# Kernel tuning notes

Hardware: AMD Instinct MI355X
Metric: run time of the kernel (lower is better)

The kernel has to match this reference:

```python
import jax, jax.numpy as jnp
import numpy as np

N = 50000
E = 800000
F_IN = 128
HID = 64
HEADS = 4
P = 16384


def setup_inputs() -> dict:
    key = jax.random.key(0)
    ks = jax.random.split(key, 20)
    s = 0.05
    inp = {
        'x': jax.random.normal(ks[0], (N, F_IN), jnp.float32),
        'edge_src': jax.random.randint(ks[1], (E,), 0, N, jnp.int32),
        'edge_dst': jax.random.randint(ks[2], (E,), 0, N, jnp.int32),
        'edge_attr': jax.random.uniform(ks[3], (E, 1), jnp.float32),
        'pair_indices': jax.random.randint(ks[4], (P, 2), 0, N, jnp.int32),
        # conv1: in=F_IN, heads=4, out=HID, edge_dim=1
        'W1': jax.random.normal(ks[5], (F_IN, HEADS * HID), jnp.float32) * s,
        'We1': jax.random.normal(ks[6], (1, HEADS * HID), jnp.float32) * s,
        'as1': jax.random.normal(ks[7], (HEADS, HID), jnp.float32) * s,
        'ad1': jax.random.normal(ks[8], (HEADS, HID), jnp.float32) * s,
        'ae1': jax.random.normal(ks[9], (HEADS, HID), jnp.float32) * s,
        'b1': jnp.zeros((HEADS * HID,), jnp.float32),
        # conv2: in=4*HID, heads=1, out=HID
        'W2': jax.random.normal(ks[10], (HEADS * HID, HID), jnp.float32) * s,
        'We2': jax.random.normal(ks[11], (1, HID), jnp.float32) * s,
        'as2': jax.random.normal(ks[12], (1, HID), jnp.float32) * s,
        'ad2': jax.random.normal(ks[13], (1, HID), jnp.float32) * s,
        'ae2': jax.random.normal(ks[14], (1, HID), jnp.float32) * s,
        'b2': jnp.zeros((HID,), jnp.float32),
        'Wlin': jax.random.normal(ks[15], (2 * HID, 1), jnp.float32) * s,
        'blin': jnp.zeros((1,), jnp.float32),
    }
    return inp


def gat_conv(x, src, dst, edge_attr, W, We, att_src, att_dst, att_edge, bias, heads, C):
    """PyG GATConv (add_self_loops=True, fill_value='mean', negative_slope=0.2, eval mode)."""
    n = x.shape[0]
    # self-loop edge_attr = mean of incoming edge attrs per node
    deg = jax.ops.segment_sum(jnp.ones_like(dst, dtype=edge_attr.dtype), dst, num_segments=n)
    loop_attr = jax.ops.segment_sum(edge_attr, dst, num_segments=n) / jnp.maximum(deg, 1.0)[:, None]
    loop = jnp.arange(n, dtype=src.dtype)
    src_f = jnp.concatenate([src, loop])
    dst_f = jnp.concatenate([dst, loop])
    ea = jnp.concatenate([edge_attr, loop_attr], axis=0)  # [E+N, 1]
    h = (x @ W).reshape(n, heads, C)                      # [N, H, C]
    a_src = (h * att_src).sum(-1)                         # [N, H]
    a_dst = (h * att_dst).sum(-1)
    e = (ea @ We).reshape(-1, heads, C)                   # [E+N, H, C]
    a_edge = (e * att_edge).sum(-1)                       # [E+N, H]
    alpha = jax.nn.leaky_relu(a_src[src_f] + a_dst[dst_f] + a_edge, 0.2)
    amax = jax.ops.segment_max(alpha, dst_f, num_segments=n)
    ex = jnp.exp(alpha - amax[dst_f])
    denom = jax.ops.segment_sum(ex, dst_f, num_segments=n)
    w = ex / denom[dst_f]                                 # segment softmax over dst
    msg = h[src_f] * w[..., None]                         # [E+N, H, C]
    out = jax.ops.segment_sum(msg, dst_f, num_segments=n) # [N, H, C]
    return out.reshape(n, heads * C) + bias


def reference(x, edge_src, edge_dst, edge_attr, pair_indices,
              W1, We1, as1, ad1, ae1, b1,
              W2, We2, as2, ad2, ae2, b2, Wlin, blin):
    # dropout is identity in eval mode
    h1 = jax.nn.elu(gat_conv(x, edge_src, edge_dst, edge_attr,
                             W1, We1, as1, ad1, ae1, b1, HEADS, HID))
    h2 = gat_conv(h1, edge_src, edge_dst, edge_attr,
                  W2, We2, as2, ad2, ae2, b2, 1, HID)
    d1 = h2[pair_indices[:, 0]]
    d2 = h2[pair_indices[:, 1]]
    pf = jnp.concatenate([d1, d2], axis=1)                # [P, 2*HID]
    return jax.nn.sigmoid(pf @ Wlin + blin).reshape(-1)
```

## Files before the change

### kernel.cpp

```cpp
#include <hip/hip_runtime.h>
#include <hip/hip_fp16.h>
#include <math.h>

typedef __attribute__((ext_vector_type(8))) short short8;
typedef __attribute__((ext_vector_type(4))) float floatx4;
typedef __attribute__((ext_vector_type(2))) float float2v;

#define LOG2E 1.4426950408889634f

__device__ __forceinline__ unsigned short f2bf(float f){
  unsigned int x = __float_as_uint(f);
  unsigned int r = x + 0x7fff + ((x >> 16) & 1);
  return (unsigned short)(r >> 16);
}
__device__ __forceinline__ unsigned char f2fp8(float v){
  int pk = __builtin_amdgcn_cvt_pk_fp8_f32(v, 0.f, 0, false);
  return (unsigned char)(pk & 0xff);
}
__device__ __forceinline__ float wsumf(float v){
#pragma unroll
  for (int o = 32; o; o >>= 1) v += __shfl_xor(v, o, 64);
  return v;
}

__global__ __launch_bounds__(256) void k_count(const int* __restrict__ dst,
    const float* __restrict__ eattr, unsigned* __restrict__ degp,
    unsigned char* __restrict__ rank, int E, int N){
  int e0 = blockIdx.x * 512 + threadIdx.x;
  int e1 = e0 + 256;
  bool v0 = e0 < E, v1 = e1 < E;
  int d0 = 0, d1 = 0; float a0 = 0.f, a1 = 0.f;
  if (v0){ d0 = dst[e0]; a0 = eattr[e0]; }
  if (v1){ d1 = dst[e1]; a1 = eattr[e1]; }
  int b0 = (e0 >> 8) & 7, b1 = (e1 >> 8) & 7;
  if (v0){
    unsigned old = atomicAdd(&degp[(size_t)b0 * N + d0],
                             (1u << 24) | (unsigned)(a0 * 262144.0f));
    rank[e0] = (unsigned char)(old >> 24);
  }
  if (v1){
    unsigned old = atomicAdd(&degp[(size_t)b1 * N + d1],
                             (1u << 24) | (unsigned)(a1 * 262144.0f));
    rank[e1] = (unsigned char)(old >> 24);
  }
}

__global__ __launch_bounds__(256) void k_scan1(const unsigned* __restrict__ degp,
    int* __restrict__ row_ptr, int* __restrict__ bsum, int n){
  __shared__ int sm[2][256];
  int tid = threadIdx.x, gid = blockIdx.x * 256 + tid;
  int v = 0;
  if (gid < n){
#pragma unroll
    for (int b = 0; b < 8; b++) v += (int)(degp[(size_t)b * n + gid] >> 24);
  }
  sm[0][tid] = v; __syncthreads();
  int pin = 0;
  for (int off = 1; off < 256; off <<= 1){
    int t = sm[pin][tid];
    if (tid >= off) t += sm[pin][tid - off];
    sm[pin ^ 1][tid] = t; pin ^= 1; __syncthreads();
  }
  int incl = sm[pin][tid];
  if (gid < n) row_ptr[gid] = incl - v;
  if (tid == 255) bsum[blockIdx.x] = incl;
}

__global__ __launch_bounds__(256) void k_scan3(int* __restrict__ row_ptr,
    const int* __restrict__ bsum, const unsigned* __restrict__ degp,
    float* __restrict__ lattr, int* __restrict__ base, int n, int E){
  int tid = threadIdx.x;
  int partial = (tid < (int)blockIdx.x) ? bsum[tid] : 0;
#pragma unroll
  for (int o = 32; o; o >>= 1) partial += __shfl_xor(partial, o, 64);
  __shared__ int ws[4];
  if ((tid & 63) == 0) ws[tid >> 6] = partial;
  __syncthreads();
  int blockOfs = ws[0] + ws[1] + ws[2] + ws[3];
  int gid = blockIdx.x * 256 + tid;
  if (gid >= n) return;
  int rp = row_ptr[gid] + blockOfs;
  row_ptr[gid] = rp;
  int cum = 0; float s = 0.f;
  int bb[8];
#pragma unroll
  for (int b = 0; b < 8; b++){
    unsigned p = degp[(size_t)b * n + gid];
    bb[b] = rp + cum;
    cum += (int)(p >> 24);
    s += (float)(p & 0xffffffu);
  }
  lattr[gid] = (s * (1.0f / 262144.0f)) / fmaxf((float)cum, 1.0f);
  int4* bp = (int4*)(base + (size_t)gid * 8);
  bp[0] = make_int4(bb[0], bb[1], bb[2], bb[3]);
  bp[1] = make_int4(bb[4], bb[5], bb[6], bb[7]);
  if (gid == 0) row_ptr[n] = E;
}

__global__ __launch_bounds__(256) void k_scatter(const int* __restrict__ src,
    const int* __restrict__ dst, const float* __restrict__ eattr,
    const unsigned char* __restrict__ rank, const int* __restrict__ base,
    int2* __restrict__ csr, int E){
  int e0 = blockIdx.x * 512 + threadIdx.x;
  int e1 = e0 + 256;
  bool v0 = e0 < E, v1 = e1 < E;
  int b0 = (e0 >> 8) & 7, b1 = (e1 >> 8) & 7;
  if (v0){
    int d = dst[e0];
    int pos = base[(size_t)d * 8 + b0] + (int)rank[e0];
    csr[pos] = make_int2(src[e0], __float_as_int(eattr[e0]));
  }
  if (v1){
    int d = dst[e1];
    int pos = base[(size_t)d * 8 + b1] + (int)rank[e1];
    csr[pos] = make_int2(src[e1], __float_as_int(eattr[e1]));
  }
}

__global__ void k_prep(const float* __restrict__ W1, const float* __restrict__ as1,
    const float* __restrict__ ad1, const float* __restrict__ W2,
    const float* __restrict__ as2, const float* __restrict__ ad2,
    const float* __restrict__ We1, const float* __restrict__ ae1,
    const float* __restrict__ We2, const float* __restrict__ ae2,
    const float* __restrict__ b2, const float* __restrict__ Wlin,
    unsigned short* __restrict__ W1p, float* __restrict__ w2vT,
    float* __restrict__ ce){
  int b = blockIdx.x, lane = threadIdx.x;
  if (b < 68){
    int nt = b >> 2, kc = b & 3;
    int col = lane & 15, krow = kc * 32 + (lane >> 4) * 8;
    unsigned short tmp[8];
    if (nt < 16){
#pragma unroll
      for (int j = 0; j < 8; j++) tmp[j] = f2bf(W1[(size_t)(krow + j) * 256 + nt * 16 + col]);
    } else {
#pragma unroll
      for (int j = 0; j < 8; j++){
        float v = 0.f;
        if (col < 8){
          const float* av = (col < 4) ? as1 : ad1;
          int h = col & 3;
          for (int c = 0; c < 64; c++)
            v += W1[(size_t)(krow + j) * 256 + h * 64 + c] * av[h * 64 + c];
          v *= LOG2E;
        }
        tmp[j] = f2bf(v);
      }
    }
    unsigned short* dstp = W1p + (((size_t)nt * 4 + kc) * 64 + lane) * 8;
    *(ushort4*)(dstp)     = make_ushort4(tmp[0], tmp[1], tmp[2], tmp[3]);
    *(ushort4*)(dstp + 4) = make_ushort4(tmp[4], tmp[5], tmp[6], tmp[7]);
  } else if (b < 72){
    int k = (b - 68) * 64 + lane;
    float4 a = make_float4(0.f, 0.f, 0.f, 0.f);
    for (int c = 0; c < 64; c++){
      float wv = W2[(size_t)k * 64 + c];
      a.x += wv * as2[c];
      a.y += wv * ad2[c];
      a.z += wv * Wlin[c];
      a.w += wv * Wlin[64 + c];
    }
    w2vT[k]       = a.x * LOG2E;
    w2vT[256 + k] = a.y * LOG2E;
    w2vT[512 + k] = a.z;
    w2vT[768 + k] = a.w;
  } else {
    float p0 = We1[lane]       * ae1[lane];
    float p1 = We1[64 + lane]  * ae1[64 + lane];
    float p2 = We1[128 + lane] * ae1[128 + lane];
    float p3 = We1[192 + lane] * ae1[192 + lane];
    float p4 = We2[lane]       * ae2[lane];
    float c1 = b2[lane] * Wlin[lane];
    float c2 = b2[lane] * Wlin[64 + lane];
    p0 = wsumf(p0); p1 = wsumf(p1); p2 = wsumf(p2); p3 = wsumf(p3); p4 = wsumf(p4);
    c1 = wsumf(c1); c2 = wsumf(c2);
    if (lane == 0){
      ce[0] = p0 * LOG2E; ce[1] = p1 * LOG2E; ce[2] = p2 * LOG2E; ce[3] = p3 * LOG2E;
      ce[4] = p4 * LOG2E;
      ce[5] = c1; ce[6] = c2;
    }
  }
}

__global__ __launch_bounds__(256) void k_gemm1_att(const float* __restrict__ A,
    const unsigned short* __restrict__ Bp, unsigned char* __restrict__ h1f8,
    float* __restrict__ asrc, float* __restrict__ adst, int M){
  constexpr int K = 128, NKC = 4;
  __shared__ unsigned short Bs[256 * K];
  {
    const uint4* srcp = (const uint4*)Bp;
    uint4* dstp = (uint4*)Bs;
    for (int i = threadIdx.x; i < 4096; i += 256) dstp[i] = srcp[i];
  }
  __syncthreads();
  int wave = threadIdx.x >> 6, lane = threadIdx.x & 63;
  int quad = lane >> 4, col = lane & 15;
  int r0 = (blockIdx.x * 4 + wave) * 16;
  int rowc = min(r0 + col, M - 1);
  short8 af[NKC], sf[NKC];
#pragma unroll
  for (int kc = 0; kc < NKC; kc++){
    float4 a0 = *(const float4*)(A + (size_t)rowc * K + kc * 32 + quad * 8);
    float4 a1 = *(const float4*)(A + (size_t)rowc * K + kc * 32 + quad * 8 + 4);
    short8 t;
    t[0] = (short)f2bf(a0.x); t[1] = (short)f2bf(a0.y);
    t[2] = (short)f2bf(a0.z); t[3] = (short)f2bf(a0.w);
    t[4] = (short)f2bf(a1.x); t[5] = (short)f2bf(a1.y);
    t[6] = (short)f2bf(a1.z); t[7] = (short)f2bf(a1.w);
    af[kc] = t;
    sf[kc] = *(const short8*)(Bp + (((size_t)16 * 4 + kc) * 64 + lane) * 8);
  }
  floatx4 acc[17];
#pragma unroll
  for (int nt = 0; nt < 17; nt++) acc[nt] = (floatx4){0.f, 0.f, 0.f, 0.f};
#pragma unroll
  for (int kc = 0; kc < NKC; kc++){
#pragma unroll
    for (int nt = 0; nt < 16; nt++){
      short8 bfv = *(const short8*)(&Bs[((nt * NKC + kc) * 64 + lane) * 8]);
      acc[nt] = __builtin_amdgcn_mfma_f32_16x16x32_bf16(af[kc], bfv, acc[nt], 0, 0, 0);
    }
    acc[16] = __builtin_amdgcn_mfma_f32_16x16x32_bf16(af[kc], sf[kc], acc[16], 0, 0, 0);
  }
#pragma unroll
  for (int nt = 0; nt < 16; nt++){
#pragma unroll
    for (int i = 0; i < 4; i++){
      int r = r0 + quad * 4 + i;
      if (r < M) h1f8[(size_t)r * 256 + nt * 16 + col] = f2fp8(acc[nt][i]);
    }
  }
#pragma unroll
  for (int i = 0; i < 4; i++){
    int r = r0 + quad * 4 + i;
    if (r < M){
      float v = acc[16][i];
      if (col < 4)      asrc[(size_t)r * 4 + col] = v;
      else if (col < 8) adst[(size_t)r * 4 + (col - 4)] = v;
    }
  }
}

__global__ __launch_bounds__(256) void k_gat1(
    const int* __restrict__ row_ptr, const int2* __restrict__ csr,
    const float* __restrict__ lattr,
    const float* __restrict__ a_src, const float* __restrict__ a_dst,
    const float* __restrict__ ce, const unsigned char* __restrict__ hpre,
    const float* __restrict__ bias, const float* __restrict__ w2vT,
    float4* __restrict__ upd, int n){
  int node = blockIdx.x * 4 + (threadIdx.x >> 6);
  if (node >= n) return;
  int lane = threadIdx.x & 63;
  int q = lane >> 4, lsub = lane & 15, hq = lsub >> 2;
  int start = row_ptr[node], deg = row_ptr[node + 1] - start;
  float4 as4 = *(const float4*)(a_src + (size_t)node * 4);
  float4 ad4 = *(const float4*)(a_dst + (size_t)node * 4);
  float4 ce4 = *(const float4*)ce;
  float la = lattr[node];
  float asvh = hq == 0 ? as4.x : hq == 1 ? as4.y : hq == 2 ? as4.z : as4.w;
  float advh = hq == 0 ? ad4.x : hq == 1 ? ad4.y : hq == 2 ? ad4.z : ad4.w;
  float ceh  = hq == 0 ? ce4.x : hq == 1 ? ce4.y : hq == 2 ? ce4.z : ce4.w;
  unsigned lso = (unsigned)(lsub << 4);
  float2v acc2[8];
#pragma unroll
  for (int k = 0; k < 8; k++) acc2[k] = (float2v){0.f, 0.f};
  float dn = 0.f;
  if (q == 0){
    float aself = fmaf(la, ceh, asvh + advh);
    aself = aself > 0.f ? aself : 0.2f * aself;
    float wself = __builtin_amdgcn_exp2f(aself);
    dn = wself;
    uint4 u = *(const uint4*)(hpre + (((unsigned)node << 8) + lso));
    float2v w2 = (float2v){wself, wself};
    unsigned uu[4] = {u.x, u.y, u.z, u.w};
#pragma unroll
    for (int j = 0; j < 4; j++){
      acc2[2 * j]     = w2 * __builtin_amdgcn_cvt_pk_f32_fp8((int)uu[j], false);
      acc2[2 * j + 1] = w2 * __builtin_amdgcn_cvt_pk_f32_fp8((int)uu[j], true);
    }
  }
  for (int e = q; e < deg; e += 16){
    int p1 = e + 4, p2 = e + 8, p3 = e + 12;
    bool v1 = p1 < deg, v2 = p2 < deg, v3 = p3 < deg;
    int2 s0 = csr[start + e];
    int2 s1 = csr[start + (v1 ? p1 : e)];
    int2 s2 = csr[start + (v2 ? p2 : e)];
    int2 s3 = csr[start + (v3 ? p3 : e)];
    uint4 u0 = *(const uint4*)(hpre + (((unsigned)s0.x << 8) + lso));
    uint4 u1 = *(const uint4*)(hpre + (((unsigned)s1.x << 8) + lso));
    uint4 u2 = *(const uint4*)(hpre + (((unsigned)s2.x << 8) + lso));
    uint4 u3 = *(const uint4*)(hpre + (((unsigned)s3.x << 8) + lso));
    float g0 = a_src[((unsigned)s0.x << 2) + hq];
    float g1 = a_src[((unsigned)s1.x << 2) + hq];
    float g2 = a_src[((unsigned)s2.x << 2) + hq];
    float g3 = a_src[((unsigned)s3.x << 2) + hq];
    float a0 = fmaf(__int_as_float(s0.y), ceh, g0 + advh);
    float a1 = fmaf(__int_as_float(s1.y), ceh, g1 + advh);
    float a2 = fmaf(__int_as_float(s2.y), ceh, g2 + advh);
    float a3 = fmaf(__int_as_float(s3.y), ceh, g3 + advh);
    a0 = a0 > 0.f ? a0 : 0.2f * a0;
    a1 = a1 > 0.f ? a1 : 0.2f * a1;
    a2 = a2 > 0.f ? a2 : 0.2f * a2;
    a3 = a3 > 0.f ? a3 : 0.2f * a3;
    float w0 = __builtin_amdgcn_exp2f(a0);
    float w1 = v1 ? __builtin_amdgcn_exp2f(a1) : 0.f;
    float w2 = v2 ? __builtin_amdgcn_exp2f(a2) : 0.f;
    float w3 = v3 ? __builtin_amdgcn_exp2f(a3) : 0.f;
    dn += (w0 + w1) + (w2 + w3);
    float2v W0 = (float2v){w0, w0}, W1 = (float2v){w1, w1};
    float2v W2 = (float2v){w2, w2}, W3 = (float2v){w3, w3};
    unsigned q0[4] = {u0.x, u0.y, u0.z, u0.w};
    unsigned q1[4] = {u1.x, u1.y, u1.z, u1.w};
    unsigned q2[4] = {u2.x, u2.y, u2.z, u2.w};
    unsigned q3[4] = {u3.x, u3.y, u3.z, u3.w};
#pragma unroll
    for (int j = 0; j < 4; j++){
      acc2[2 * j]     += W0 * __builtin_amdgcn_cvt_pk_f32_fp8((int)q0[j], false);
      acc2[2 * j + 1] += W0 * __builtin_amdgcn_cvt_pk_f32_fp8((int)q0[j], true);
      acc2[2 * j]     += W1 * __builtin_amdgcn_cvt_pk_f32_fp8((int)q1[j], false);
      acc2[2 * j + 1] += W1 * __builtin_amdgcn_cvt_pk_f32_fp8((int)q1[j], true);
      acc2[2 * j]     += W2 * __builtin_amdgcn_cvt_pk_f32_fp8((int)q2[j], false);
      acc2[2 * j + 1] += W2 * __builtin_amdgcn_cvt_pk_f32_fp8((int)q2[j], true);
      acc2[2 * j]     += W3 * __builtin_amdgcn_cvt_pk_f32_fp8((int)q3[j], false);
      acc2[2 * j + 1] += W3 * __builtin_amdgcn_cvt_pk_f32_fp8((int)q3[j], true);
    }
  }
  dn += __shfl_xor(dn, 16, 64);
  dn += __shfl_xor(dn, 32, 64);
#pragma unroll
  for (int k = 0; k < 8; k++){
    acc2[k].x += __shfl_xor(acc2[k].x, 16, 64);
    acc2[k].x += __shfl_xor(acc2[k].x, 32, 64);
    acc2[k].y += __shfl_xor(acc2[k].y, 16, 64);
    acc2[k].y += __shfl_xor(acc2[k].y, 32, 64);
  }
  {
    float inv = 1.f / dn;
    float d = 0.f;
#pragma unroll
    for (int j = 0; j < 4; j++){
      float4 b4  = *(const float4*)(bias + lsub * 16 + j * 4);
      float4 wvj = *(const float4*)(w2vT + (size_t)lane * 16 + j * 4);
      float bbv[4] = {b4.x, b4.y, b4.z, b4.w};
      float wvv[4] = {wvj.x, wvj.y, wvj.z, wvj.w};
#pragma unroll
      for (int t = 0; t < 4; t++){
        int k = j * 4 + t;
        float av = (k & 1) ? acc2[k >> 1].y : acc2[k >> 1].x;
        float v = av * inv + bbv[t];
        v = v > 0.f ? v : (__expf(v) - 1.f);
        d += v * wvv[t];
      }
    }
#pragma unroll
    for (int o = 1; o < 16; o <<= 1) d += __shfl_xor(d, o, 64);
    if (lsub == 0) ((float*)&upd[node])[q] = d;
  }
}

__global__ __launch_bounds__(256) void k_gat2(
    const int* __restrict__ row_ptr, const int2* __restrict__ csr,
    const float* __restrict__ lattr, const float4* __restrict__ upd,
    const float* __restrict__ ce,
    float* __restrict__ s1v, float* __restrict__ s2v, int n){
  int node = blockIdx.x * 32 + (threadIdx.x >> 3);
  if (node >= n) return;
  int lane8 = threadIdx.x & 7;
  int start = row_ptr[node], deg = row_ptr[node + 1] - start;
  float4 own = upd[node];
  float ad = own.y, c = ce[4];
  const float* updf = (const float*)upd;
  float t1 = 0.f, t2 = 0.f, dn = 0.f;
  if (lane8 == 0){
    float a = fmaf(lattr[node], c, own.x + ad);
    a = a > 0.f ? a : 0.2f * a;
    float w = __builtin_amdgcn_exp2f(a);
    dn = w; t1 = w * own.z; t2 = w * own.w;
  }
  for (int e = lane8; e < deg; e += 16){
    bool vB = (e + 8) < deg;
    int2 sA = csr[start + e];
    int2 sB = csr[start + (vB ? e + 8 : e)];
    float4 oA = *(const float4*)(updf + ((unsigned)sA.x << 2));
    float4 oB = *(const float4*)(updf + ((unsigned)sB.x << 2));
    float aA = fmaf(__int_as_float(sA.y), c, oA.x + ad);
    float aB = fmaf(__int_as_float(sB.y), c, oB.x + ad);
    aA = aA > 0.f ? aA : 0.2f * aA;
    aB = aB > 0.f ? aB : 0.2f * aB;
    float wA = __builtin_amdgcn_exp2f(aA);
    float wB = vB ? __builtin_amdgcn_exp2f(aB) : 0.f;
    dn += wA + wB;
    t1 = fmaf(wA, oA.z, fmaf(wB, oB.z, t1));
    t2 = fmaf(wA, oA.w, fmaf(wB, oB.w, t2));
  }
#pragma unroll
  for (int o = 1; o < 8; o <<= 1){
    dn += __shfl_xor(dn, o, 64);
    t1 += __shfl_xor(t1, o, 64);
    t2 += __shfl_xor(t2, o, 64);
  }
  if (lane8 == 0){
    float inv = 1.f / dn;
    s1v[node] = t1 * inv + ce[5];
    s2v[node] = t2 * inv + ce[6];
  }
}

__global__ __launch_bounds__(256) void k_pairs(const int* __restrict__ pairs,
    const float* __restrict__ s1v, const float* __restrict__ s2v,
    const float* __restrict__ blin, float* __restrict__ out, int P){
  int p = blockIdx.x * 256 + threadIdx.x;
  if (p >= P) return;
  int i = pairs[2 * p], j = pairs[2 * p + 1];
  float x = s1v[i] + s2v[j] + blin[0];
  out[p] = 1.f / (1.f + __expf(-x));
}

extern "C" void kernel_launch(void* const* d_in, const int* in_sizes, int n_in,
                              void* d_out, int out_size, void* d_ws, size_t ws_size,
                              hipStream_t stream) {
  const float* x     = (const float*)d_in[0];
  const int*   esrc  = (const int*)  d_in[1];
  const int*   edst  = (const int*)  d_in[2];
  const float* eattr = (const float*)d_in[3];
  const int*   pairs = (const int*)  d_in[4];
  const float* W1    = (const float*)d_in[5];
  const float* We1   = (const float*)d_in[6];
  const float* as1   = (const float*)d_in[7];
  const float* ad1   = (const float*)d_in[8];
  const float* ae1   = (const float*)d_in[9];
  const float* b1    = (const float*)d_in[10];
  const float* W2    = (const float*)d_in[11];
  const float* We2   = (const float*)d_in[12];
  const float* as2   = (const float*)d_in[13];
  const float* ad2   = (const float*)d_in[14];
  const float* ae2   = (const float*)d_in[15];
  const float* b2    = (const float*)d_in[16];
  const float* Wlin  = (const float*)d_in[17];
  const float* blin  = (const float*)d_in[18];
  float* out = (float*)d_out;

  const int N = in_sizes[0] / 128;
  const int E = in_sizes[1];
  const int P = in_sizes[4] / 2;

  char* w = (char*)d_ws;
  size_t off = 0;
  auto alloc = [&](size_t bytes) -> size_t {
    size_t r = off; off = (off + bytes + 255) & ~(size_t)255; return r;
  };
  size_t o_degp   = alloc((size_t)N * 32);
  size_t zero_end = off;
  size_t o_rank   = alloc((size_t)E);
  size_t o_rowptr = alloc((size_t)(N + 1) * 4);
  size_t o_bsum   = alloc(1024);
  size_t o_lattr  = alloc((size_t)N * 4);
  size_t o_base   = alloc((size_t)N * 32);
  size_t o_csr    = alloc((size_t)E * 8);
  size_t o_asrc1  = alloc((size_t)N * 16);
  size_t o_adst1  = alloc((size_t)N * 16);
  size_t o_upd    = alloc((size_t)N * 16);
  size_t o_ce     = alloc(64);
  size_t o_s1     = alloc((size_t)N * 4);
  size_t o_s2     = alloc((size_t)N * 4);
  size_t o_W1p    = alloc((size_t)17 * 4 * 64 * 8 * 2);
  size_t o_w2v    = alloc(256 * 16);
  size_t o_h1f8   = alloc((size_t)N * 256);
  (void)ws_size;

  unsigned* degp = (unsigned*)(w + o_degp);
  unsigned char* rank = (unsigned char*)(w + o_rank);
  int*   rowptr = (int*)  (w + o_rowptr);
  int*   bsum   = (int*)  (w + o_bsum);
  float* lattr  = (float*)(w + o_lattr);
  int*   base   = (int*)  (w + o_base);
  int2*  csr    = (int2*) (w + o_csr);
  float* asrc1  = (float*)(w + o_asrc1);
  float* adst1  = (float*)(w + o_adst1);
  float4* upd   = (float4*)(w + o_upd);
  float* ce     = (float*)(w + o_ce);
  float* s1v    = (float*)(w + o_s1);
  float* s2v    = (float*)(w + o_s2);
  unsigned short* W1p = (unsigned short*)(w + o_W1p);
  float* w2vT   = (float*)(w + o_w2v);
  unsigned char* h1f8 = (unsigned char*)(w + o_h1f8);

  hipMemsetAsync(w, 0, zero_end, stream);

  int ebl2 = (E + 511) / 512;
  int nbl = (N + 255) / 256;
  int wbl = (N + 3) / 4;

  k_count<<<ebl2, 256, 0, stream>>>(edst, eattr, degp, rank, E, N);
  k_scan1<<<nbl, 256, 0, stream>>>(degp, rowptr, bsum, N);
  k_scan3<<<nbl, 256, 0, stream>>>(rowptr, bsum, degp, lattr, base, N, E);
  k_scatter<<<ebl2, 256, 0, stream>>>(esrc, edst, eattr, rank, base, csr, E);

  k_prep<<<73, 64, 0, stream>>>(W1, as1, ad1, W2, as2, ad2,
                                We1, ae1, We2, ae2, b2, Wlin, W1p, w2vT, ce);

  k_gemm1_att<<<(N + 63) / 64, 256, 0, stream>>>(x, W1p, h1f8, asrc1, adst1, N);
  k_gat1<<<wbl, 256, 0, stream>>>(rowptr, csr, lattr, asrc1, adst1, ce,
                                  h1f8, b1, w2vT, upd, N);
  k_gat2<<<(N + 31) / 32, 256, 0, stream>>>(rowptr, csr, lattr, upd, ce,
                                            s1v, s2v, N);
  k_pairs<<<(P + 255) / 256, 256, 0, stream>>>(pairs, s1v, s2v, blin, out, P);
}
```

Baseline: 256.4 us.

## Fuse graph-build kernels with prep/GEMM and embed fp16 source attention in CSR

The edge count kernel now shares one launch with weight preprocessing, and the first scan shares one launch with the layer-1 GEMM. This removes two launches and lets independent work run concurrently. The scatter now runs after the GEMM and packs each edge's four per-head source attention logits as fp16 into a widened 16-byte CSR entry. That lets gat1 skip a random a_src gather, and its edge loop is reduced from 4-way to 2-way unroll. In exchange the CSR is twice as large, which gat2 also reads, and source attention logits lose precision to fp16.

```diff
diff --git a/kernel.cpp b/kernel.cpp
--- a/kernel.cpp
+++ b/kernel.cpp
@@ -22,102 +22,20 @@
   for (int o = 32; o; o >>= 1) v += __shfl_xor(v, o, 64);
   return v;
 }
-
-__global__ __launch_bounds__(256) void k_count(const int* __restrict__ dst,
+__device__ __forceinline__ unsigned pkh2(float a, float b){
+  auto p = __builtin_amdgcn_cvt_pkrtz(a, b);
+  unsigned u; __builtin_memcpy(&u, &p, 4); return u;
+}
+__device__ __forceinline__ float h2f(unsigned v){
+  unsigned short us = (unsigned short)v;
+  __fp16 h; __builtin_memcpy(&h, &us, 2);
+  return (float)h;
+}
+
+__global__ __launch_bounds__(256) void k_count_prep(const int* __restrict__ dst,
     const float* __restrict__ eattr, unsigned* __restrict__ degp,
-    unsigned char* __restrict__ rank, int E, int N){
-  int e0 = blockIdx.x * 512 + threadIdx.x;
-  int e1 = e0 + 256;
-  bool v0 = e0 < E, v1 = e1 < E;
-  int d0 = 0, d1 = 0; float a0 = 0.f, a1 = 0.f;
-  if (v0){ d0 = dst[e0]; a0 = eattr[e0]; }
-  if (v1){ d1 = dst[e1]; a1 = eattr[e1]; }
-  int b0 = (e0 >> 8) & 7, b1 = (e1 >> 8) & 7;
-  if (v0){
-    unsigned old = atomicAdd(&degp[(size_t)b0 * N + d0],
-                             (1u << 24) | (unsigned)(a0 * 262144.0f));
-    rank[e0] = (unsigned char)(old >> 24);
-  }
-  if (v1){
-    unsigned old = atomicAdd(&degp[(size_t)b1 * N + d1],
-                             (1u << 24) | (unsigned)(a1 * 262144.0f));
-    rank[e1] = (unsigned char)(old >> 24);
-  }
-}
-
-__global__ __launch_bounds__(256) void k_scan1(const unsigned* __restrict__ degp,
-    int* __restrict__ row_ptr, int* __restrict__ bsum, int n){
-  __shared__ int sm[2][256];
-  int tid = threadIdx.x, gid = blockIdx.x * 256 + tid;
-  int v = 0;
-  if (gid < n){
-#pragma unroll
-    for (int b = 0; b < 8; b++) v += (int)(degp[(size_t)b * n + gid] >> 24);
-  }
-  sm[0][tid] = v; __syncthreads();
-  int pin = 0;
-  for (int off = 1; off < 256; off <<= 1){
-    int t = sm[pin][tid];
-    if (tid >= off) t += sm[pin][tid - off];
-    sm[pin ^ 1][tid] = t; pin ^= 1; __syncthreads();
-  }
-  int incl = sm[pin][tid];
-  if (gid < n) row_ptr[gid] = incl - v;
-  if (tid == 255) bsum[blockIdx.x] = incl;
-}
-
-__global__ __launch_bounds__(256) void k_scan3(int* __restrict__ row_ptr,
-    const int* __restrict__ bsum, const unsigned* __restrict__ degp,
-    float* __restrict__ lattr, int* __restrict__ base, int n, int E){
-  int tid = threadIdx.x;
-  int partial = (tid < (int)blockIdx.x) ? bsum[tid] : 0;
-#pragma unroll
-  for (int o = 32; o; o >>= 1) partial += __shfl_xor(partial, o, 64);
-  __shared__ int ws[4];
-  if ((tid & 63) == 0) ws[tid >> 6] = partial;
-  __syncthreads();
-  int blockOfs = ws[0] + ws[1] + ws[2] + ws[3];
-  int gid = blockIdx.x * 256 + tid;
-  if (gid >= n) return;
-  int rp = row_ptr[gid] + blockOfs;
-  row_ptr[gid] = rp;
-  int cum = 0; float s = 0.f;
-  int bb[8];
-#pragma unroll
-  for (int b = 0; b < 8; b++){
-    unsigned p = degp[(size_t)b * n + gid];
-    bb[b] = rp + cum;
-    cum += (int)(p >> 24);
-    s += (float)(p & 0xffffffu);
-  }
-  lattr[gid] = (s * (1.0f / 262144.0f)) / fmaxf((float)cum, 1.0f);
-  int4* bp = (int4*)(base + (size_t)gid * 8);
-  bp[0] = make_int4(bb[0], bb[1], bb[2], bb[3]);
-  bp[1] = make_int4(bb[4], bb[5], bb[6], bb[7]);
-  if (gid == 0) row_ptr[n] = E;
-}
-
-__global__ __launch_bounds__(256) void k_scatter(const int* __restrict__ src,
-    const int* __restrict__ dst, const float* __restrict__ eattr,
-    const unsigned char* __restrict__ rank, const int* __restrict__ base,
-    int2* __restrict__ csr, int E){
-  int e0 = blockIdx.x * 512 + threadIdx.x;
-  int e1 = e0 + 256;
-  bool v0 = e0 < E, v1 = e1 < E;
-  int b0 = (e0 >> 8) & 7, b1 = (e1 >> 8) & 7;
-  if (v0){
-    int d = dst[e0];
-    int pos = base[(size_t)d * 8 + b0] + (int)rank[e0];
-    csr[pos] = make_int2(src[e0], __float_as_int(eattr[e0]));
-  }
-  if (v1){
-    int d = dst[e1];
-    int pos = base[(size_t)d * 8 + b1] + (int)rank[e1];
-    csr[pos] = make_int2(src[e1], __float_as_int(eattr[e1]));
-  }
-}
-
-__global__ void k_prep(const float* __restrict__ W1, const float* __restrict__ as1,
+    unsigned char* __restrict__ rank, int E, int N, int ebl2,
+    const float* __restrict__ W1, const float* __restrict__ as1,
     const float* __restrict__ ad1, const float* __restrict__ W2,
     const float* __restrict__ as2, const float* __restrict__ ad2,
     const float* __restrict__ We1, const float* __restrict__ ae1,
@@ -125,7 +43,28 @@
     const float* __restrict__ b2, const float* __restrict__ Wlin,
     unsigned short* __restrict__ W1p, float* __restrict__ w2vT,
     float* __restrict__ ce){
-  int b = blockIdx.x, lane = threadIdx.x;
+  if ((int)blockIdx.x < ebl2){
+    int e0 = blockIdx.x * 512 + threadIdx.x;
+    int e1 = e0 + 256;
+    bool v0 = e0 < E, v1 = e1 < E;
+    int d0 = 0, d1 = 0; float a0 = 0.f, a1 = 0.f;
+    if (v0){ d0 = dst[e0]; a0 = eattr[e0]; }
+    if (v1){ d1 = dst[e1]; a1 = eattr[e1]; }
+    int b0 = (e0 >> 8) & 7, b1 = (e1 >> 8) & 7;
+    if (v0){
+      unsigned old = atomicAdd(&degp[(size_t)b0 * N + d0],
+                               (1u << 24) | (unsigned)(a0 * 262144.0f));
+      rank[e0] = (unsigned char)(old >> 24);
+    }
+    if (v1){
+      unsigned old = atomicAdd(&degp[(size_t)b1 * N + d1],
+                               (1u << 24) | (unsigned)(a1 * 262144.0f));
+      rank[e1] = (unsigned char)(old >> 24);
+    }
+    return;
+  }
+  if (threadIdx.x >= 64) return;
+  int b = blockIdx.x - ebl2, lane = threadIdx.x;
   if (b < 68){
     int nt = b >> 2, kc = b & 3;
     int col = lane & 15, krow = kc * 32 + (lane >> 4) * 8;
@@ -182,11 +121,35 @@
   }
 }
 
-__global__ __launch_bounds__(256) void k_gemm1_att(const float* __restrict__ A,
-    const unsigned short* __restrict__ Bp, unsigned char* __restrict__ h1f8,
-    float* __restrict__ asrc, float* __restrict__ adst, int M){
+__global__ __launch_bounds__(256) void k_scan1_gemm(
+    const unsigned* __restrict__ degp, int* __restrict__ row_ptr,
+    int* __restrict__ bsum, int n, int gbl,
+    const float* __restrict__ A, const unsigned short* __restrict__ Bp,
+    unsigned char* __restrict__ h1f8, float* __restrict__ asrc,
+    float* __restrict__ adst, int M){
+  __shared__ unsigned short Bs[256 * 128];
+  if ((int)blockIdx.x >= gbl){
+    int* sm = (int*)Bs;
+    int sb = blockIdx.x - gbl;
+    int tid = threadIdx.x, gid = sb * 256 + tid;
+    int v = 0;
+    if (gid < n){
+#pragma unroll
+      for (int b = 0; b < 8; b++) v += (int)(degp[(size_t)b * n + gid] >> 24);
+    }
+    sm[tid] = v; __syncthreads();
+    int pin = 0;
+    for (int off = 1; off < 256; off <<= 1){
+      int t = sm[pin * 256 + tid];
+      if (tid >= off) t += sm[pin * 256 + tid - off];
+      sm[(pin ^ 1) * 256 + tid] = t; pin ^= 1; __syncthreads();
+    }
+    int incl = sm[pin * 256 + tid];
+    if (gid < n) row_ptr[gid] = incl - v;
+    if (tid == 255) bsum[sb] = incl;
+    return;
+  }
   constexpr int K = 128, NKC = 4;
-  __shared__ unsigned short Bs[256 * K];
   {
     const uint4* srcp = (const uint4*)Bp;
     uint4* dstp = (uint4*)Bs;
@@ -241,8 +204,63 @@
   }
 }
 
+__global__ __launch_bounds__(256) void k_scan3(int* __restrict__ row_ptr,
+    const int* __restrict__ bsum, const unsigned* __restrict__ degp,
+    float* __restrict__ lattr, int* __restrict__ base, int n, int E){
+  int tid = threadIdx.x;
+  int partial = (tid < (int)blockIdx.x) ? bsum[tid] : 0;
+#pragma unroll
+  for (int o = 32; o; o >>= 1) partial += __shfl_xor(partial, o, 64);
+  __shared__ int ws[4];
+  if ((tid & 63) == 0) ws[tid >> 6] = partial;
+  __syncthreads();
+  int blockOfs = ws[0] + ws[1] + ws[2] + ws[3];
+  int gid = blockIdx.x * 256 + tid;
+  if (gid >= n) return;
+  int rp = row_ptr[gid] + blockOfs;
+  row_ptr[gid] = rp;
+  int cum = 0; float s = 0.f;
+  int bb[8];
+#pragma unroll
+  for (int b = 0; b < 8; b++){
+    unsigned p = degp[(size_t)b * n + gid];
+    bb[b] = rp + cum;
+    cum += (int)(p >> 24);
+    s += (float)(p & 0xffffffu);
+  }
+  lattr[gid] = (s * (1.0f / 262144.0f)) / fmaxf((float)cum, 1.0f);
+  int4* bp = (int4*)(base + (size_t)gid * 8);
+  bp[0] = make_int4(bb[0], bb[1], bb[2], bb[3]);
+  bp[1] = make_int4(bb[4], bb[5], bb[6], bb[7]);
+  if (gid == 0) row_ptr[n] = E;
+}
+
+__global__ __launch_bounds__(256) void k_scatter(const int* __restrict__ src,
+    const int* __restrict__ dst, const float* __restrict__ eattr,
+    const unsigned char* __restrict__ rank, const int* __restrict__ base,
+    const float* __restrict__ a_src, int4* __restrict__ csr, int E){
+  int e0 = blockIdx.x * 512 + threadIdx.x;
+  int e1 = e0 + 256;
+  bool v0 = e0 < E, v1 = e1 < E;
+  int b0 = (e0 >> 8) & 7, b1 = (e1 >> 8) & 7;
+  if (v0){
+    int d = dst[e0], s = src[e0];
+    int pos = base[(size_t)d * 8 + b0] + (int)rank[e0];
+    float4 av = *(const float4*)(a_src + ((size_t)s << 2));
+    csr[pos] = make_int4(s, __float_as_int(eattr[e0]),
+                         (int)pkh2(av.x, av.y), (int)pkh2(av.z, av.w));
+  }
+  if (v1){
+    int d = dst[e1], s = src[e1];
+    int pos = base[(size_t)d * 8 + b1] + (int)rank[e1];
+    float4 av = *(const float4*)(a_src + ((size_t)s << 2));
+    csr[pos] = make_int4(s, __float_as_int(eattr[e1]),
+                         (int)pkh2(av.x, av.y), (int)pkh2(av.z, av.w));
+  }
+}
+
 __global__ __launch_bounds__(256) void k_gat1(
-    const int* __restrict__ row_ptr, const int2* __restrict__ csr,
+    const int* __restrict__ row_ptr, const int4* __restrict__ csr,
     const float* __restrict__ lattr,
     const float* __restrict__ a_src, const float* __restrict__ a_dst,
     const float* __restrict__ ce, const unsigned char* __restrict__ hpre,
@@ -261,6 +279,7 @@
   float advh = hq == 0 ? ad4.x : hq == 1 ? ad4.y : hq == 2 ? ad4.z : ad4.w;
   float ceh  = hq == 0 ? ce4.x : hq == 1 ? ce4.y : hq == 2 ? ce4.z : ce4.w;
   unsigned lso = (unsigned)(lsub << 4);
+  int hsh = (hq & 1) * 16;
   float2v acc2[8];
 #pragma unroll
   for (int k = 0; k < 8; k++) acc2[k] = (float2v){0.f, 0.f};
@@ -279,50 +298,32 @@
       acc2[2 * j + 1] = w2 * __builtin_amdgcn_cvt_pk_f32_fp8((int)uu[j], true);
     }
   }
-  for (int e = q; e < deg; e += 16){
-    int p1 = e + 4, p2 = e + 8, p3 = e + 12;
-    bool v1 = p1 < deg, v2 = p2 < deg, v3 = p3 < deg;
-    int2 s0 = csr[start + e];
-    int2 s1 = csr[start + (v1 ? p1 : e)];
-    int2 s2 = csr[start + (v2 ? p2 : e)];
-    int2 s3 = csr[start + (v3 ? p3 : e)];
-    uint4 u0 = *(const uint4*)(hpre + (((unsigned)s0.x << 8) + lso));
-    uint4 u1 = *(const uint4*)(hpre + (((unsigned)s1.x << 8) + lso));
-    uint4 u2 = *(const uint4*)(hpre + (((unsigned)s2.x << 8) + lso));
-    uint4 u3 = *(const uint4*)(hpre + (((unsigned)s3.x << 8) + lso));
-    float g0 = a_src[((unsigned)s0.x << 2) + hq];
-    float g1 = a_src[((unsigned)s1.x << 2) + hq];
-    float g2 = a_src[((unsigned)s2.x << 2) + hq];
-    float g3 = a_src[((unsigned)s3.x << 2) + hq];
-    float a0 = fmaf(__int_as_float(s0.y), ceh, g0 + advh);
-    float a1 = fmaf(__int_as_float(s1.y), ceh, g1 + advh);
-    float a2 = fmaf(__int_as_float(s2.y), ceh, g2 + advh);
-    float a3 = fmaf(__int_as_float(s3.y), ceh, g3 + advh);
-    a0 = a0 > 0.f ? a0 : 0.2f * a0;
-    a1 = a1 > 0.f ? a1 : 0.2f * a1;
-    a2 = a2 > 0.f ? a2 : 0.2f * a2;
-    a3 = a3 > 0.f ? a3 : 0.2f * a3;
-    float w0 = __builtin_amdgcn_exp2f(a0);
-    float w1 = v1 ? __builtin_amdgcn_exp2f(a1) : 0.f;
-    float w2 = v2 ? __builtin_amdgcn_exp2f(a2) : 0.f;
-    float w3 = v3 ? __builtin_amdgcn_exp2f(a3) : 0.f;
-    dn += (w0 + w1) + (w2 + w3);
-    float2v W0 = (float2v){w0, w0}, W1 = (float2v){w1, w1};
-    float2v W2 = (float2v){w2, w2}, W3 = (float2v){w3, w3};
-    unsigned q0[4] = {u0.x, u0.y, u0.z, u0.w};
-    unsigned q1[4] = {u1.x, u1.y, u1.z, u1.w};
-    unsigned q2[4] = {u2.x, u2.y, u2.z, u2.w};
-    unsigned q3[4] = {u3.x, u3.y, u3.z, u3.w};
+  for (int e = q; e < deg; e += 8){
+    bool vB = (e + 4) < deg;
+    int4 sA = csr[start + e];
+    int4 sB = csr[start + (vB ? e + 4 : e)];
+    uint4 uA = *(const uint4*)(hpre + (((unsigned)sA.x << 8) + lso));
+    uint4 uB = *(const uint4*)(hpre + (((unsigned)sB.x << 8) + lso));
+    unsigned hwA = (hq & 2) ? (unsigned)sA.w : (unsigned)sA.z;
+    unsigned hwB = (hq & 2) ? (unsigned)sB.w : (unsigned)sB.z;
+    float gA = h2f(hwA >> hsh);
+    float gB = h2f(hwB >> hsh);
+    float aA = fmaf(__int_as_float(sA.y), ceh, gA + advh);
+    float aB = fmaf(__int_as_float(sB.y), ceh, gB + advh);
+    aA = aA > 0.f ? aA : 0.2f * aA;
+    aB = aB > 0.f ? aB : 0.2f * aB;
+    float wA = __builtin_amdgcn_exp2f(aA);
+    float wB = vB ? __builtin_amdgcn_exp2f(aB) : 0.f;
+    dn += wA + wB;
+    float2v wA2 = (float2v){wA, wA}, wB2 = (float2v){wB, wB};
+    unsigned ua[4] = {uA.x, uA.y, uA.z, uA.w};
+    unsigned ub[4] = {uB.x, uB.y, uB.z, uB.w};
 #pragma unroll
     for (int j = 0; j < 4; j++){
-      acc2[2 * j]     += W0 * __builtin_amdgcn_cvt_pk_f32_fp8((int)q0[j], false);
-      acc2[2 * j + 1] += W0 * __builtin_amdgcn_cvt_pk_f32_fp8((int)q0[j], true);
-      acc2[2 * j]     += W1 * __builtin_amdgcn_cvt_pk_f32_fp8((int)q1[j], false);
-      acc2[2 * j + 1] += W1 * __builtin_amdgcn_cvt_pk_f32_fp8((int)q1[j], true);
-      acc2[2 * j]     += W2 * __builtin_amdgcn_cvt_pk_f32_fp8((int)q2[j], false);
-      acc2[2 * j + 1] += W2 * __builtin_amdgcn_cvt_pk_f32_fp8((int)q2[j], true);
-      acc2[2 * j]     += W3 * __builtin_amdgcn_cvt_pk_f32_fp8((int)q3[j], false);
-      acc2[2 * j + 1] += W3 * __builtin_amdgcn_cvt_pk_f32_fp8((int)q3[j], true);
+      acc2[2 * j]     += wA2 * __builtin_amdgcn_cvt_pk_f32_fp8((int)ua[j], false);
+      acc2[2 * j + 1] += wA2 * __builtin_amdgcn_cvt_pk_f32_fp8((int)ua[j], true);
+      acc2[2 * j]     += wB2 * __builtin_amdgcn_cvt_pk_f32_fp8((int)ub[j], false);
+      acc2[2 * j + 1] += wB2 * __builtin_amdgcn_cvt_pk_f32_fp8((int)ub[j], true);
     }
   }
   dn += __shfl_xor(dn, 16, 64);
@@ -359,7 +360,7 @@
 }
 
 __global__ __launch_bounds__(256) void k_gat2(
-    const int* __restrict__ row_ptr, const int2* __restrict__ csr,
+    const int* __restrict__ row_ptr, const int4* __restrict__ csr,
     const float* __restrict__ lattr, const float4* __restrict__ upd,
     const float* __restrict__ ce,
     float* __restrict__ s1v, float* __restrict__ s2v, int n){
@@ -379,8 +380,8 @@
   }
   for (int e = lane8; e < deg; e += 16){
     bool vB = (e + 8) < deg;
-    int2 sA = csr[start + e];
-    int2 sB = csr[start + (vB ? e + 8 : e)];
+    int4 sA = csr[start + e];
+    int4 sB = csr[start + (vB ? e + 8 : e)];
     float4 oA = *(const float4*)(updf + ((unsigned)sA.x << 2));
     float4 oB = *(const float4*)(updf + ((unsigned)sB.x << 2));
     float aA = fmaf(__int_as_float(sA.y), c, oA.x + ad);
@@ -456,7 +457,7 @@
   size_t o_bsum   = alloc(1024);
   size_t o_lattr  = alloc((size_t)N * 4);
   size_t o_base   = alloc((size_t)N * 32);
-  size_t o_csr    = alloc((size_t)E * 8);
+  size_t o_csr    = alloc((size_t)E * 16);
   size_t o_asrc1  = alloc((size_t)N * 16);
   size_t o_adst1  = alloc((size_t)N * 16);
   size_t o_upd    = alloc((size_t)N * 16);
@@ -474,7 +475,7 @@
   int*   bsum   = (int*)  (w + o_bsum);
   float* lattr  = (float*)(w + o_lattr);
   int*   base   = (int*)  (w + o_base);
-  int2*  csr    = (int2*) (w + o_csr);
+  int4*  csr    = (int4*) (w + o_csr);
   float* asrc1  = (float*)(w + o_asrc1);
   float* adst1  = (float*)(w + o_adst1);
   float4* upd   = (float4*)(w + o_upd);
@@ -485,21 +486,19 @@
   float* w2vT   = (float*)(w + o_w2v);
   unsigned char* h1f8 = (unsigned char*)(w + o_h1f8);
 
-  hipMemsetAsync(w, 0, zero_end, stream);
+  (void)hipMemsetAsync(w, 0, zero_end, stream);
 
   int ebl2 = (E + 511) / 512;
   int nbl = (N + 255) / 256;
+  int gbl = (N + 63) / 64;
   int wbl = (N + 3) / 4;
 
-  k_count<<<ebl2, 256, 0, stream>>>(edst, eattr, degp, rank, E, N);
-  k_scan1<<<nbl, 256, 0, stream>>>(degp, rowptr, bsum, N);
+  k_count_prep<<<ebl2 + 73, 256, 0, stream>>>(edst, eattr, degp, rank, E, N, ebl2,
+      W1, as1, ad1, W2, as2, ad2, We1, ae1, We2, ae2, b2, Wlin, W1p, w2vT, ce);
+  k_scan1_gemm<<<gbl + nbl, 256, 0, stream>>>(degp, rowptr, bsum, N, gbl,
+      x, W1p, h1f8, asrc1, adst1, N);
   k_scan3<<<nbl, 256, 0, stream>>>(rowptr, bsum, degp, lattr, base, N, E);
-  k_scatter<<<ebl2, 256, 0, stream>>>(esrc, edst, eattr, rank, base, csr, E);
-
-  k_prep<<<73, 64, 0, stream>>>(W1, as1, ad1, W2, as2, ad2,
-                                We1, ae1, We2, ae2, b2, Wlin, W1p, w2vT, ce);
-
-  k_gemm1_att<<<(N + 63) / 64, 256, 0, stream>>>(x, W1p, h1f8, asrc1, adst1, N);
+  k_scatter<<<ebl2, 256, 0, stream>>>(esrc, edst, eattr, rank, base, asrc1, csr, E);
   k_gat1<<<wbl, 256, 0, stream>>>(rowptr, csr, lattr, asrc1, adst1, ce,
                                   h1f8, b1, w2vT, upd, N);
   k_gat2<<<(N + 31) / 32, 256, 0, stream>>>(rowptr, csr, lattr, upd, ce,
```

Measured after the change: 250.1 us. 1.03x faster.
